# Kernel tuning notes

Hardware: AMD Instinct MI355X
Metric: run time of the kernel (lower is better)

The kernel has to match this reference:

```python
import jax, jax.numpy as jnp
import numpy as np

D_MODEL = 1024
N_HEADS = 16
HEAD_DIM = 64
SEQ = 2048
BATCH = 2
NEG = -1e9


def rotate_half(t):
    t1, t2 = jnp.split(t, 2, axis=-1)
    return jnp.concatenate([-t2, t1], axis=-1)


def setup_inputs() -> dict:
    key = jax.random.key(0)
    ks = jax.random.split(key, 7)
    std = 0.02
    x = jax.random.normal(ks[0], (BATCH, SEQ, D_MODEL), dtype=jnp.float32)
    # RoPE tables [seq_len, head_dim]
    inv_freq = 1.0 / (10000.0 ** (jnp.arange(0, HEAD_DIM, 2, dtype=jnp.float32) / HEAD_DIM))
    t = jnp.arange(SEQ, dtype=jnp.float32)
    freqs = jnp.outer(t, inv_freq)
    emb = jnp.concatenate([freqs, freqs], axis=-1)
    cos = jnp.cos(emb)
    sin = jnp.sin(emb)
    Wq = std * jax.random.normal(ks[1], (D_MODEL, D_MODEL), dtype=jnp.float32)
    Wk = std * jax.random.normal(ks[2], (D_MODEL, D_MODEL), dtype=jnp.float32)
    Wv = std * jax.random.normal(ks[3], (D_MODEL, D_MODEL), dtype=jnp.float32)
    Wo = std * jax.random.normal(ks[4], (D_MODEL, D_MODEL), dtype=jnp.float32)
    return {"x": x, "cos": cos, "sin": sin, "Wq": Wq, "Wk": Wk, "Wv": Wv, "Wo": Wo}


def reference(x, cos, sin, Wq, Wk, Wv, Wo):
    B, S, _ = x.shape
    scale = 1.0 / np.sqrt(HEAD_DIM)
    # projections (nn.Linear: y = x @ W.T)
    q = (x @ Wq.T).reshape(B, S, N_HEADS, HEAD_DIM).transpose(0, 2, 1, 3)  # [B,H,S,D]
    k = (x @ Wk.T).reshape(B, S, N_HEADS, HEAD_DIM).transpose(0, 2, 1, 3)
    v = (x @ Wv.T).reshape(B, S, N_HEADS, HEAD_DIM).transpose(0, 2, 1, 3)
    # RoPE
    c = cos[None, None, :, :]
    s = sin[None, None, :, :]
    q = q * c + rotate_half(q) * s
    k = k * c + rotate_half(k) * s
    # attention with additive causal mask
    scores = jnp.einsum('bhqd,bhkd->bhqk', q, k) * scale
    causal = jnp.triu(jnp.ones((S, S), dtype=jnp.float32), k=1) * NEG
    scores = scores + causal[None, None]
    attn = jax.nn.softmax(scores, axis=-1)
    out = jnp.einsum('bhqk,bhkd->bhqd', attn, v)
    out = out.transpose(0, 2, 1, 3).reshape(B, S, D_MODEL)
    return out @ Wo.T
```

## Files before the change

kernel.cpp:

```cpp
#include <hip/hip_runtime.h>
#include <hip/hip_bf16.h>
#include <math.h>

#define DM    1024
#define SEQL  2048
#define NB    2
#define MTOT  4096
#define NTAB  (SEQL * 64)

typedef __attribute__((ext_vector_type(8))) short short8;
typedef __attribute__((ext_vector_type(4))) short short4v;
typedef __attribute__((ext_vector_type(4))) float float4v;

#define GLDS16(g, l) __builtin_amdgcn_global_load_lds( \
    (const __attribute__((address_space(1))) void*)(g), \
    (__attribute__((address_space(3))) void*)(l), 16, 0, 0)

__device__ __forceinline__ short f2bf(float f) {
  union { float f; unsigned u; } c; c.f = f;
  unsigned r = c.u + 0x7FFFu + ((c.u >> 16) & 1u);
  return (short)(r >> 16);
}

__device__ __forceinline__ int packbf(float a, float b) {
  union { float f; unsigned u; } ca, cb; ca.f = a; cb.f = b;
  return (int)__builtin_amdgcn_perm(cb.u + 0x8000u, ca.u + 0x8000u, 0x07060302u);
}

__device__ __forceinline__ float bflo(unsigned u) {
  union { unsigned u; float f; } c; c.u = u << 16; return c.f;
}
__device__ __forceinline__ float bfhi(unsigned u) {
  union { unsigned u; float f; } c; c.u = u & 0xFFFF0000u; return c.f;
}

__global__ __launch_bounds__(256) void cvt_all(
    const float* __restrict__ x, const float* __restrict__ wq, const float* __restrict__ wk,
    const float* __restrict__ wv, const float* __restrict__ wo,
    const float* __restrict__ cosp, const float* __restrict__ sinp,
    short* __restrict__ xb, short* __restrict__ wqb, short* __restrict__ wkb,
    short* __restrict__ wvb, short* __restrict__ wob,
    unsigned* __restrict__ csq, unsigned* __restrict__ csk) {
  const int n4x = MTOT * DM / 4;
  const int n4all = n4x + DM * DM;
  int i = blockIdx.x * 256 + threadIdx.x;
  if (i < n4all) {
    const float* s; short* d; int off;
    if (i < n4x) { s = x; d = xb; off = i; }
    else {
      int j = i - n4x;
      int sel = j >> 18;
      off = j & 0x3FFFF;
      s = (sel == 0) ? wq : (sel == 1) ? wk : (sel == 2) ? wv : wo;
      d = (sel == 0) ? wqb : (sel == 1) ? wkb : (sel == 2) ? wvb : wob;
    }
    float4 v = ((const float4*)s)[off];
    short4v o;
    o.x = f2bf(v.x); o.y = f2bf(v.y); o.z = f2bf(v.z); o.w = f2bf(v.w);
    ((short4v*)d)[off] = o;
  } else {
    int j2 = i - n4all;
    if (j2 < NTAB) {
      const float sc = 0.18033688011112042f;
      float c = cosp[j2], s = sinp[j2];
      csq[j2] = (unsigned)packbf(c * sc, s * sc);
      csk[j2] = (unsigned)packbf(c, s);
    }
  }
}

__global__ __launch_bounds__(256, 3) void qkv_kernel(
    const short* __restrict__ A,
    const short* __restrict__ B0, const short* __restrict__ B1, const short* __restrict__ B2,
    short* __restrict__ out0, short* __restrict__ out1, short* __restrict__ out2,
    const unsigned* __restrict__ csq, const unsigned* __restrict__ csk)
{
  __shared__ short As[2][128 * 32];
  __shared__ short Bs[2][128 * 32];
  const int t = threadIdx.x;
  const int w = t >> 6, lane = t & 63;
  const int quad = lane >> 4, l16 = lane & 15;
  const int wm = w >> 1, wn = w & 1;
  const int bm = blockIdx.y * 128, bn = blockIdx.x * 128;
  const int pA = (l16 + (l16 >> 2)) & 3;

  const short* Bw = (blockIdx.z == 0) ? B0 : ((blockIdx.z == 1) ? B1 : B2);

  float4v acc[4][4];
#pragma unroll
  for (int i = 0; i < 4; ++i)
#pragma unroll
    for (int j = 0; j < 4; ++j) { float4v z = {0.f, 0.f, 0.f, 0.f}; acc[i][j] = z; }

  auto stage = [&](int k0, int p) {
#pragma unroll
    for (int i = 0; i < 2; ++i) {
      const int idx = i * 256 + t;
      const int row = idx >> 2;
      const int g = (idx & 3) ^ ((row + (row >> 2)) & 3);
      GLDS16(A  + (size_t)(bm + row) * DM + k0 + g * 8, &As[p][(i * 256 + w * 64) * 8]);
      GLDS16(Bw + (size_t)(bn + row) * DM + k0 + g * 8, &Bs[p][(i * 256 + w * 64) * 8]);
    }
  };

  stage(0, 0);
  for (int ki = 0; ki < 32; ++ki) {
    const int p = ki & 1;
    __syncthreads();
    if (ki < 31) stage((ki + 1) * 32, p ^ 1);
    short8 af[4], bf[4];
#pragma unroll
    for (int mt = 0; mt < 4; ++mt)
      af[mt] = *(const short8*)&As[p][(wm * 64 + mt * 16 + l16) * 32 + ((quad ^ pA)) * 8];
#pragma unroll
    for (int nt = 0; nt < 4; ++nt)
      bf[nt] = *(const short8*)&Bs[p][(wn * 64 + nt * 16 + l16) * 32 + ((quad ^ pA)) * 8];
#pragma unroll
    for (int mt = 0; mt < 4; ++mt)
#pragma unroll
      for (int nt = 0; nt < 4; ++nt)
        acc[mt][nt] = __builtin_amdgcn_mfma_f32_16x16x32_bf16(af[mt], bf[nt], acc[mt][nt], 0, 0, 0);
  }

  if (blockIdx.z < 2) {
    short* qo = (blockIdx.z == 0) ? out0 : out1;
    const unsigned* tbl = (blockIdx.z == 0) ? csq : csk;
#pragma unroll
    for (int mt = 0; mt < 4; ++mt)
#pragma unroll
      for (int r = 0; r < 4; ++r) {
        int grow = bm + wm * 64 + mt * 16 + quad * 4 + r;
        int s = grow & (SEQL - 1);
        int base = grow * DM + bn + wn * 64;
#pragma unroll
        for (int nt = 0; nt < 2; ++nt) {
          int d1 = nt * 16 + l16;
          float q1 = acc[mt][nt][r], q2 = acc[mt][nt + 2][r];
          unsigned t0 = tbl[s * 64 + d1];
          unsigned t1 = tbl[s * 64 + 32 + d1];
          qo[base + d1]      = f2bf(q1 * bflo(t0) - q2 * bfhi(t0));
          qo[base + 32 + d1] = f2bf(q2 * bflo(t1) + q1 * bfhi(t1));
        }
      }
  } else {
    short* vo = out2;
#pragma unroll
    for (int mt = 0; mt < 4; ++mt)
#pragma unroll
      for (int nt = 0; nt < 4; ++nt) {
        int gc = bn + wn * 64 + nt * 16 + l16;
        int g0 = bm + wm * 64 + mt * 16 + quad * 4;
        short4v pk;
#pragma unroll
        for (int r = 0; r < 4; ++r) pk[r] = f2bf(acc[mt][nt][r]);
        *(short4v*)&vo[(size_t)gc * MTOT + g0] = pk;
      }
  }
}

__global__ __launch_bounds__(512, 4) void attn_kernel(
    const short* __restrict__ Q, const short* __restrict__ K,
    const short* __restrict__ Vt, short* __restrict__ O)
{
  __shared__ short smem[34816];
  short* Ks = smem;
  short* Vs = smem + 8192;
  const int t = threadIdx.x;
  const int wid = t >> 6, lane = t & 63;
  const int quad = lane >> 4, l16 = lane & 15;
  const int g = wid >> 2;
  const int qg = wid & 3;
  short* Pl = smem + 16384 + wid * (2 * 16 * 72);
  const int qtA = blockIdx.x, qtB = 31 - blockIdx.x;
  const int bh = blockIdx.y, b = bh >> 4, h = bh & 15;
  const int rowbase = b * SEQL, colbase = h * 64;
  const int nktA = (qtA >> 1) + 1, nktB = (qtB >> 1) + 1;
  const int qA = qtA * 64 + qg * 16 + l16;
  const int qB = qtB * 64 + qg * 16 + l16;

  short8 aqA[2], aqB[2];
#pragma unroll
  for (int kk = 0; kk < 2; ++kk) {
    aqA[kk] = *(const short8*)&Q[(size_t)(rowbase + qA) * DM + colbase + kk * 32 + quad * 8];
    aqB[kk] = *(const short8*)&Q[(size_t)(rowbase + qB) * DM + colbase + kk * 32 + quad * 8];
  }

  float4v oA[4], oB[4];
#pragma unroll
  for (int j = 0; j < 4; ++j) { float4v z = {0.f, 0.f, 0.f, 0.f}; oA[j] = z; oB[j] = z; }
  float lA = 0.f, lB = 0.f;

  for (int kt = 0; kt < nktB; ++kt) {
    {
      const short* Kbase = K + (size_t)(rowbase + kt * 128) * DM + colbase;
      const short* Vbase = Vt + (size_t)colbase * MTOT + rowbase + kt * 128;
#pragma unroll
      for (int j = 0; j < 2; ++j) {
        int i = j * 512 + t;
        int n = i >> 3, c = (i & 7) ^ (n & 7);
        GLDS16(Kbase + (size_t)n * DM + c * 8, Ks + (j * 512 + wid * 64) * 8);
      }
#pragma unroll
      for (int j = 0; j < 2; ++j) {
        int i = j * 512 + t;
        int d = i >> 4, c = (i & 15) ^ (d & 7);
        GLDS16(Vbase + (size_t)d * MTOT + c * 8, Vs + (j * 512 + wid * 64) * 8);
      }
    }
    __syncthreads();
    const bool actA = (kt < nktA);
    const bool diagA = (kt == nktA - 1), diagB = (kt == nktB - 1);

#pragma unroll
    for (int ntl = 0; ntl < 4; ++ntl) {
      const int nt = g * 4 + ntl;
      const int n = nt * 16 + l16;
      short8 bk0 = *(const short8*)&Ks[(n * 8 + (quad ^ (n & 7))) * 8];
      short8 bk1 = *(const short8*)&Ks[(n * 8 + ((4 + quad) ^ (n & 7))) * 8];
      const int kb = kt * 128 + nt * 16 + quad * 4;
      float4v zz = {0.f, 0.f, 0.f, 0.f};
      float4v sB = __builtin_amdgcn_mfma_f32_16x16x32_bf16(bk0, aqB[0], zz, 0, 0, 0);
      sB = __builtin_amdgcn_mfma_f32_16x16x32_bf16(bk1, aqB[1], sB, 0, 0, 0);
      float pb[4];
#pragma unroll
      for (int r = 0; r < 4; ++r) {
        float pv = (diagB && (kb + r > qB)) ? 0.f : __builtin_amdgcn_exp2f(sB[r]);
        lB += pv; pb[r] = pv;
      }
      *(int2*)&Pl[1 * 16 * 72 + l16 * 72 + ntl * 16 + quad * 4] =
          make_int2(packbf(pb[0], pb[1]), packbf(pb[2], pb[3]));
      if (actA) {
        float4v sA = __builtin_amdgcn_mfma_f32_16x16x32_bf16(bk0, aqA[0], zz, 0, 0, 0);
        sA = __builtin_amdgcn_mfma_f32_16x16x32_bf16(bk1, aqA[1], sA, 0, 0, 0);
        float pa[4];
#pragma unroll
        for (int r = 0; r < 4; ++r) {
          float pv = (diagA && (kb + r > qA)) ? 0.f : __builtin_amdgcn_exp2f(sA[r]);
          lA += pv; pa[r] = pv;
        }
        *(int2*)&Pl[0 * 16 * 72 + l16 * 72 + ntl * 16 + quad * 4] =
            make_int2(packbf(pa[0], pa[1]), packbf(pa[2], pa[3]));
      }
    }

#pragma unroll
    for (int kk = 0; kk < 2; ++kk) {
      short8 apB = *(const short8*)&Pl[1 * 16 * 72 + l16 * 72 + kk * 32 + quad * 8];
      short8 apA;
      if (actA) apA = *(const short8*)&Pl[0 * 16 * 72 + l16 * 72 + kk * 32 + quad * 8];
      const int c0 = g * 8 + kk * 4 + quad;
#pragma unroll
      for (int dt = 0; dt < 4; ++dt) {
        const int d = dt * 16 + l16;
        short8 bv = *(const short8*)&Vs[(d * 16 + (c0 ^ (d & 7))) * 8];
        oB[dt] = __builtin_amdgcn_mfma_f32_16x16x32_bf16(apB, bv, oB[dt], 0, 0, 0);
        if (actA) oA[dt] = __builtin_amdgcn_mfma_f32_16x16x32_bf16(apA, bv, oA[dt], 0, 0, 0);
      }
    }
    __syncthreads();
  }

  lA += __shfl_xor(lA, 16); lA += __shfl_xor(lA, 32);
  lB += __shfl_xor(lB, 16); lB += __shfl_xor(lB, 32);

  __syncthreads();
  float* Ored = (float*)smem;
  float* Lred = (float*)smem + 8448;
  if (g == 1) {
#pragma unroll
    for (int tile = 0; tile < 2; ++tile) {
      const float4v* src = (tile == 0) ? oA : oB;
      const int base = ((tile * 4 + qg) * 16) * 66;
#pragma unroll
      for (int dt = 0; dt < 4; ++dt)
#pragma unroll
        for (int r = 0; r < 4; ++r)
          Ored[base + (quad * 4 + r) * 66 + dt * 16 + l16] = src[dt][r];
    }
    if (lane < 16) {
      Lred[(0 * 4 + qg) * 16 + l16] = lA;
      Lred[(1 * 4 + qg) * 16 + l16] = lB;
    }
  }
  __syncthreads();
  if (g == 0) {
    const float tA = lA + Lred[(0 * 4 + qg) * 16 + l16];
    const float tB = lB + Lred[(1 * 4 + qg) * 16 + l16];
    float iAr[4], iBr[4];
#pragma unroll
    for (int r = 0; r < 4; ++r) {
      iAr[r] = 1.f / __shfl(tA, quad * 4 + r);
      iBr[r] = 1.f / __shfl(tB, quad * 4 + r);
    }
#pragma unroll
    for (int tile = 0; tile < 2; ++tile) {
      const float4v* src = (tile == 0) ? oA : oB;
      const int qt = (tile == 0) ? qtA : qtB;
      const int base = ((tile * 4 + qg) * 16) * 66;
#pragma unroll
      for (int dt = 0; dt < 4; ++dt)
#pragma unroll
        for (int r = 0; r < 4; ++r) {
          float v = src[dt][r] + Ored[base + (quad * 4 + r) * 66 + dt * 16 + l16];
          int grow = rowbase + qt * 64 + qg * 16 + quad * 4 + r;
          int gcol = colbase + dt * 16 + l16;
          O[(size_t)grow * DM + gcol] = f2bf(v * ((tile == 0) ? iAr[r] : iBr[r]));
        }
    }
  }
}

__global__ __launch_bounds__(256, 2) void gemm_out(
    const short* __restrict__ A, const short* __restrict__ B,
    float* __restrict__ out)
{
  __shared__ short As[2][128 * 32];
  __shared__ short Bs[2][64 * 32];
  const int t = threadIdx.x;
  const int w = t >> 6, lane = t & 63;
  const int quad = lane >> 4, l16 = lane & 15;
  const int wm = w >> 1, wn = w & 1;
  const int bm = blockIdx.y * 128, bn = blockIdx.x * 64;
  const int pA = (l16 + (l16 >> 2)) & 3;

  float4v acc[4][2];
#pragma unroll
  for (int i = 0; i < 4; ++i)
#pragma unroll
    for (int j = 0; j < 2; ++j) { float4v z = {0.f, 0.f, 0.f, 0.f}; acc[i][j] = z; }

  auto stage = [&](int k0, int p) {
#pragma unroll
    for (int i = 0; i < 2; ++i) {
      const int idx = i * 256 + t;
      const int row = idx >> 2;
      const int gch = (idx & 3) ^ ((row + (row >> 2)) & 3);
      GLDS16(A + (size_t)(bm + row) * DM + k0 + gch * 8, &As[p][(i * 256 + w * 64) * 8]);
    }
    {
      const int row = t >> 2;
      const int gch = (t & 3) ^ ((row + (row >> 2)) & 3);
      GLDS16(B + (size_t)(bn + row) * DM + k0 + gch * 8, &Bs[p][(w * 64) * 8]);
    }
  };

  stage(0, 0);
  for (int ki = 0; ki < 32; ++ki) {
    const int p = ki & 1;
    __syncthreads();
    if (ki < 31) stage((ki + 1) * 32, p ^ 1);
    short8 af[4], bf[2];
#pragma unroll
    for (int mt = 0; mt < 4; ++mt)
      af[mt] = *(const short8*)&As[p][(wm * 64 + mt * 16 + l16) * 32 + ((quad ^ pA)) * 8];
#pragma unroll
    for (int nt = 0; nt < 2; ++nt)
      bf[nt] = *(const short8*)&Bs[p][(wn * 32 + nt * 16 + l16) * 32 + ((quad ^ pA)) * 8];
#pragma unroll
    for (int mt = 0; mt < 4; ++mt)
#pragma unroll
      for (int nt = 0; nt < 2; ++nt)
        acc[mt][nt] = __builtin_amdgcn_mfma_f32_16x16x32_bf16(af[mt], bf[nt], acc[mt][nt], 0, 0, 0);
  }

#pragma unroll
  for (int mt = 0; mt < 4; ++mt)
#pragma unroll
    for (int nt = 0; nt < 2; ++nt)
#pragma unroll
      for (int r = 0; r < 4; ++r) {
        int grow = bm + wm * 64 + mt * 16 + quad * 4 + r;
        int gcol = bn + wn * 32 + nt * 16 + l16;
        out[(size_t)grow * DM + gcol] = acc[mt][nt][r];
      }
}

extern "C" void kernel_launch(void* const* d_in, const int* in_sizes, int n_in,
                              void* d_out, int out_size, void* d_ws, size_t ws_size,
                              hipStream_t stream) {
  const float* x    = (const float*)d_in[0];
  const float* cosp = (const float*)d_in[1];
  const float* sinp = (const float*)d_in[2];
  const float* Wq   = (const float*)d_in[3];
  const float* Wk   = (const float*)d_in[4];
  const float* Wv   = (const float*)d_in[5];
  const float* Wo   = (const float*)d_in[6];

  char* ws = (char*)d_ws;
  const size_t XB = (size_t)MTOT * DM * 2;
  const size_t WB = (size_t)DM * DM * 2;
  short* xb    = (short*)(ws);
  short* wqb   = (short*)(ws + XB);
  short* wkb   = (short*)(ws + XB + 1 * WB);
  short* wvb   = (short*)(ws + XB + 2 * WB);
  short* wob   = (short*)(ws + XB + 3 * WB);
  short* Qb    = (short*)(ws + XB + 4 * WB);
  short* Kb    = (short*)(ws + XB + 4 * WB + XB);
  short* Vtb   = (short*)(ws + XB + 4 * WB + 2 * XB);
  unsigned* csq = (unsigned*)(ws + XB + 4 * WB + 3 * XB);
  unsigned* csk = (unsigned*)(ws + XB + 4 * WB + 3 * XB + NTAB * 4);
  short* attnb = xb;

  const int ntot = (MTOT * DM + 4 * DM * DM) / 4 + NTAB;
  hipLaunchKernelGGL(cvt_all, dim3((ntot + 255) / 256), dim3(256), 0, stream,
                     x, Wq, Wk, Wv, Wo, cosp, sinp, xb, wqb, wkb, wvb, wob, csq, csk);

  hipLaunchKernelGGL(qkv_kernel, dim3(DM / 128, MTOT / 128, 3), dim3(256), 0, stream,
                     xb, wqb, wkb, wvb, Qb, Kb, Vtb, csq, csk);

  hipLaunchKernelGGL(attn_kernel, dim3(16, NB * 16), dim3(512), 0, stream,
                     Qb, Kb, Vtb, attnb);

  hipLaunchKernelGGL(gemm_out, dim3(DM / 64, MTOT / 128), dim3(256), 0, stream,
                     attnb, wob, (float*)d_out);
}
```

Before: 181.2 us.

## Load GEMM and attention operands directly from global memory, dropping LDS staging

Removes the LDS double-buffered staging (global_load_lds plus barriers) in the QKV GEMM, the output GEMM and the attention K/V loads. Each wave now reads its MFMA fragments straight from global memory through per-row pointers. This frees LDS and drops the syncthreads, and gemm_out's occupancy hint is raised. The cost is that operands shared between waves are fetched redundantly through L1/L2 with no software prefetch, so latency hiding depends on unrolling and occupancy.

```diff
diff --git a/kernel.cpp b/kernel.cpp
--- a/kernel.cpp
+++ b/kernel.cpp
@@ -11,10 +11,6 @@
 typedef __attribute__((ext_vector_type(8))) short short8;
 typedef __attribute__((ext_vector_type(4))) short short4v;
 typedef __attribute__((ext_vector_type(4))) float float4v;
-
-#define GLDS16(g, l) __builtin_amdgcn_global_load_lds( \
-    (const __attribute__((address_space(1))) void*)(g), \
-    (__attribute__((address_space(3))) void*)(l), 16, 0, 0)
 
 __device__ __forceinline__ short f2bf(float f) {
   union { float f; unsigned u; } c; c.f = f;
@@ -75,46 +71,36 @@
     short* __restrict__ out0, short* __restrict__ out1, short* __restrict__ out2,
     const unsigned* __restrict__ csq, const unsigned* __restrict__ csk)
 {
-  __shared__ short As[2][128 * 32];
-  __shared__ short Bs[2][128 * 32];
   const int t = threadIdx.x;
   const int w = t >> 6, lane = t & 63;
   const int quad = lane >> 4, l16 = lane & 15;
   const int wm = w >> 1, wn = w & 1;
   const int bm = blockIdx.y * 128, bn = blockIdx.x * 128;
-  const int pA = (l16 + (l16 >> 2)) & 3;
 
   const short* Bw = (blockIdx.z == 0) ? B0 : ((blockIdx.z == 1) ? B1 : B2);
 
+  const short* arow[4];
+  const short* brow[4];
+#pragma unroll
+  for (int mt = 0; mt < 4; ++mt)
+    arow[mt] = A  + (size_t)(bm + wm * 64 + mt * 16 + l16) * DM + quad * 8;
+#pragma unroll
+  for (int nt = 0; nt < 4; ++nt)
+    brow[nt] = Bw + (size_t)(bn + wn * 64 + nt * 16 + l16) * DM + quad * 8;
+
   float4v acc[4][4];
 #pragma unroll
   for (int i = 0; i < 4; ++i)
 #pragma unroll
     for (int j = 0; j < 4; ++j) { float4v z = {0.f, 0.f, 0.f, 0.f}; acc[i][j] = z; }
 
-  auto stage = [&](int k0, int p) {
-#pragma unroll
-    for (int i = 0; i < 2; ++i) {
-      const int idx = i * 256 + t;
-      const int row = idx >> 2;
-      const int g = (idx & 3) ^ ((row + (row >> 2)) & 3);
-      GLDS16(A  + (size_t)(bm + row) * DM + k0 + g * 8, &As[p][(i * 256 + w * 64) * 8]);
-      GLDS16(Bw + (size_t)(bn + row) * DM + k0 + g * 8, &Bs[p][(i * 256 + w * 64) * 8]);
-    }
-  };
-
-  stage(0, 0);
-  for (int ki = 0; ki < 32; ++ki) {
-    const int p = ki & 1;
-    __syncthreads();
-    if (ki < 31) stage((ki + 1) * 32, p ^ 1);
+#pragma unroll 2
+  for (int k0 = 0; k0 < DM; k0 += 32) {
     short8 af[4], bf[4];
 #pragma unroll
-    for (int mt = 0; mt < 4; ++mt)
-      af[mt] = *(const short8*)&As[p][(wm * 64 + mt * 16 + l16) * 32 + ((quad ^ pA)) * 8];
-#pragma unroll
-    for (int nt = 0; nt < 4; ++nt)
-      bf[nt] = *(const short8*)&Bs[p][(wn * 64 + nt * 16 + l16) * 32 + ((quad ^ pA)) * 8];
+    for (int mt = 0; mt < 4; ++mt) af[mt] = *(const short8*)(arow[mt] + k0);
+#pragma unroll
+    for (int nt = 0; nt < 4; ++nt) bf[nt] = *(const short8*)(brow[nt] + k0);
 #pragma unroll
     for (int mt = 0; mt < 4; ++mt)
 #pragma unroll
@@ -162,15 +148,13 @@
     const short* __restrict__ Q, const short* __restrict__ K,
     const short* __restrict__ Vt, short* __restrict__ O)
 {
-  __shared__ short smem[34816];
-  short* Ks = smem;
-  short* Vs = smem + 8192;
+  __shared__ short smem[18432];
   const int t = threadIdx.x;
   const int wid = t >> 6, lane = t & 63;
   const int quad = lane >> 4, l16 = lane & 15;
   const int g = wid >> 2;
   const int qg = wid & 3;
-  short* Pl = smem + 16384 + wid * (2 * 16 * 72);
+  short* Pl = smem + wid * (2 * 16 * 72);
   const int qtA = blockIdx.x, qtB = 31 - blockIdx.x;
   const int bh = blockIdx.y, b = bh >> 4, h = bh & 15;
   const int rowbase = b * SEQL, colbase = h * 64;
@@ -185,38 +169,27 @@
     aqB[kk] = *(const short8*)&Q[(size_t)(rowbase + qB) * DM + colbase + kk * 32 + quad * 8];
   }
 
+  const short* krow = K + (size_t)(rowbase + (g * 4) * 16 + l16) * DM + colbase + quad * 8;
+  const short* vrow[4];
+#pragma unroll
+  for (int dt = 0; dt < 4; ++dt)
+    vrow[dt] = Vt + (size_t)(colbase + dt * 16 + l16) * MTOT + rowbase + g * 64 + quad * 8;
+
   float4v oA[4], oB[4];
 #pragma unroll
   for (int j = 0; j < 4; ++j) { float4v z = {0.f, 0.f, 0.f, 0.f}; oA[j] = z; oB[j] = z; }
   float lA = 0.f, lB = 0.f;
 
   for (int kt = 0; kt < nktB; ++kt) {
-    {
-      const short* Kbase = K + (size_t)(rowbase + kt * 128) * DM + colbase;
-      const short* Vbase = Vt + (size_t)colbase * MTOT + rowbase + kt * 128;
-#pragma unroll
-      for (int j = 0; j < 2; ++j) {
-        int i = j * 512 + t;
-        int n = i >> 3, c = (i & 7) ^ (n & 7);
-        GLDS16(Kbase + (size_t)n * DM + c * 8, Ks + (j * 512 + wid * 64) * 8);
-      }
-#pragma unroll
-      for (int j = 0; j < 2; ++j) {
-        int i = j * 512 + t;
-        int d = i >> 4, c = (i & 15) ^ (d & 7);
-        GLDS16(Vbase + (size_t)d * MTOT + c * 8, Vs + (j * 512 + wid * 64) * 8);
-      }
-    }
-    __syncthreads();
     const bool actA = (kt < nktA);
     const bool diagA = (kt == nktA - 1), diagB = (kt == nktB - 1);
 
 #pragma unroll
     for (int ntl = 0; ntl < 4; ++ntl) {
       const int nt = g * 4 + ntl;
-      const int n = nt * 16 + l16;
-      short8 bk0 = *(const short8*)&Ks[(n * 8 + (quad ^ (n & 7))) * 8];
-      short8 bk1 = *(const short8*)&Ks[(n * 8 + ((4 + quad) ^ (n & 7))) * 8];
+      const short* kp = krow + (size_t)(kt * 128 + ntl * 16) * DM;
+      short8 bk0 = *(const short8*)(kp);
+      short8 bk1 = *(const short8*)(kp + 32);
       const int kb = kt * 128 + nt * 16 + quad * 4;
       float4v zz = {0.f, 0.f, 0.f, 0.f};
       float4v sB = __builtin_amdgcn_mfma_f32_16x16x32_bf16(bk0, aqB[0], zz, 0, 0, 0);
@@ -248,16 +221,13 @@
       short8 apB = *(const short8*)&Pl[1 * 16 * 72 + l16 * 72 + kk * 32 + quad * 8];
       short8 apA;
       if (actA) apA = *(const short8*)&Pl[0 * 16 * 72 + l16 * 72 + kk * 32 + quad * 8];
-      const int c0 = g * 8 + kk * 4 + quad;
 #pragma unroll
       for (int dt = 0; dt < 4; ++dt) {
-        const int d = dt * 16 + l16;
-        short8 bv = *(const short8*)&Vs[(d * 16 + (c0 ^ (d & 7))) * 8];
+        short8 bv = *(const short8*)(vrow[dt] + kt * 128 + kk * 32);
         oB[dt] = __builtin_amdgcn_mfma_f32_16x16x32_bf16(apB, bv, oB[dt], 0, 0, 0);
         if (actA) oA[dt] = __builtin_amdgcn_mfma_f32_16x16x32_bf16(apA, bv, oA[dt], 0, 0, 0);
       }
     }
-    __syncthreads();
   }
 
   lA += __shfl_xor(lA, 16); lA += __shfl_xor(lA, 32);
@@ -310,18 +280,24 @@
   }
 }
 
-__global__ __launch_bounds__(256, 2) void gemm_out(
+__global__ __launch_bounds__(256, 3) void gemm_out(
     const short* __restrict__ A, const short* __restrict__ B,
     float* __restrict__ out)
 {
-  __shared__ short As[2][128 * 32];
-  __shared__ short Bs[2][64 * 32];
   const int t = threadIdx.x;
   const int w = t >> 6, lane = t & 63;
   const int quad = lane >> 4, l16 = lane & 15;
   const int wm = w >> 1, wn = w & 1;
   const int bm = blockIdx.y * 128, bn = blockIdx.x * 64;
-  const int pA = (l16 + (l16 >> 2)) & 3;
+
+  const short* arow[4];
+  const short* brow[2];
+#pragma unroll
+  for (int mt = 0; mt < 4; ++mt)
+    arow[mt] = A + (size_t)(bm + wm * 64 + mt * 16 + l16) * DM + quad * 8;
+#pragma unroll
+  for (int nt = 0; nt < 2; ++nt)
+    brow[nt] = B + (size_t)(bn + wn * 32 + nt * 16 + l16) * DM + quad * 8;
 
   float4v acc[4][2];
 #pragma unroll
@@ -329,33 +305,13 @@
 #pragma unroll
     for (int j = 0; j < 2; ++j) { float4v z = {0.f, 0.f, 0.f, 0.f}; acc[i][j] = z; }
 
-  auto stage = [&](int k0, int p) {
-#pragma unroll
-    for (int i = 0; i < 2; ++i) {
-      const int idx = i * 256 + t;
-      const int row = idx >> 2;
-      const int gch = (idx & 3) ^ ((row + (row >> 2)) & 3);
-      GLDS16(A + (size_t)(bm + row) * DM + k0 + gch * 8, &As[p][(i * 256 + w * 64) * 8]);
-    }
-    {
-      const int row = t >> 2;
-      const int gch = (t & 3) ^ ((row + (row >> 2)) & 3);
-      GLDS16(B + (size_t)(bn + row) * DM + k0 + gch * 8, &Bs[p][(w * 64) * 8]);
-    }
-  };
-
-  stage(0, 0);
-  for (int ki = 0; ki < 32; ++ki) {
-    const int p = ki & 1;
-    __syncthreads();
-    if (ki < 31) stage((ki + 1) * 32, p ^ 1);
+#pragma unroll 2
+  for (int k0 = 0; k0 < DM; k0 += 32) {
     short8 af[4], bf[2];
 #pragma unroll
-    for (int mt = 0; mt < 4; ++mt)
-      af[mt] = *(const short8*)&As[p][(wm * 64 + mt * 16 + l16) * 32 + ((quad ^ pA)) * 8];
-#pragma unroll
-    for (int nt = 0; nt < 2; ++nt)
-      bf[nt] = *(const short8*)&Bs[p][(wn * 32 + nt * 16 + l16) * 32 + ((quad ^ pA)) * 8];
+    for (int mt = 0; mt < 4; ++mt) af[mt] = *(const short8*)(arow[mt] + k0);
+#pragma unroll
+    for (int nt = 0; nt < 2; ++nt) bf[nt] = *(const short8*)(brow[nt] + k0);
 #pragma unroll
     for (int mt = 0; mt < 4; ++mt)
 #pragma unroll
```

New measurement: 346.4 us. +91.2%, slower.
